# Kernel optimization log

Hardware: AMD Instinct MI355X
Metric: run time of the kernel (lower is better)

The kernel has to match this reference:

```python
import jax, jax.numpy as jnp
import numpy as np

B, T, HID = 4, 2048, 1024
H, FD, HD = 16, 16, 64          # heads, feature_dim, head_dim
CHUNK = 64                      # chunk size for chunked linear attention
EPS_LN = 1e-5                   # layer-norm eps inside feature map
EPS_Z = 1e-10                   # normalize_output eps


def setup_inputs() -> dict:
    key = jax.random.key(0)
    ks = jax.random.split(key, 7)
    init = lambda k, shp: jax.random.normal(k, shp, jnp.float32) * (shp[-1] ** -0.5)
    return {
        "hidden_states": jax.random.normal(ks[0], (B, T, HID), jnp.float32),
        "Wq": init(ks[1], (H * FD, HID)),     # q_proj weight [out,in], no bias
        "Wk": init(ks[2], (H * FD, HID)),
        "Wv": init(ks[3], (H * HD, HID)),
        "Wo": init(ks[4], (H * HD, HID)),
        "gamma": jnp.ones((FD,), jnp.float32),  # RebasedFeatureMap layer-norm scale
        "beta": jnp.zeros((FD,), jnp.float32),  # RebasedFeatureMap layer-norm shift
    }


def _feature_map(x, gamma, beta):
    # layer_norm over feature_dim, then quadratic (outer-product) feature map.
    mu = x.mean(-1, keepdims=True)
    var = ((x - mu) ** 2).mean(-1, keepdims=True)
    xn = (x - mu) * jax.lax.rsqrt(var + EPS_LN) * gamma + beta
    d = xn.shape[-1]
    # [B,T,H,d] -> [B,T,H,d*d]
    x2 = (xn[..., :, None] * xn[..., None, :]).reshape(*xn.shape[:-1], d * d)
    return x2 * (d ** -0.5)


def _chunk_linear_attn(q, k, v):
    # Chunk-recurrent causal linear attention (simple GLA with no gates, scale=1).
    Bq, Tq, Hq, Kq = q.shape
    Vd = v.shape[-1]
    N = Tq // CHUNK
    # [B,T,H,D] -> [N,B,H,C,D] for scan over chunks
    to_chunks = lambda x: x.reshape(Bq, N, CHUNK, Hq, x.shape[-1]).transpose(1, 0, 3, 2, 4)
    qc, kc, vc = to_chunks(q), to_chunks(k), to_chunks(v)
    mask = jnp.tril(jnp.ones((CHUNK, CHUNK), bool))

    def step(state, xs):
        qb, kb, vb = xs  # [B,H,C,K], [B,H,C,K], [B,H,C,V]
        att = jnp.einsum('bhik,bhjk->bhij', qb, kb)
        att = jnp.where(mask, att, 0.0)
        o = jnp.einsum('bhij,bhjv->bhiv', att, vb) + jnp.einsum('bhik,bhkv->bhiv', qb, state)
        state = state + jnp.einsum('bhck,bhcv->bhkv', kb, vb)
        return state, o

    state0 = jnp.zeros((Bq, Hq, Kq, Vd), q.dtype)
    _, o = jax.lax.scan(step, state0, (qc, kc, vc))  # o: [N,B,H,C,V]
    o = o.transpose(1, 0, 3, 2, 4).reshape(Bq, Tq, Hq, Vd)
    # normalize_output: z_t = q_t . cumsum_{s<=t} k_s
    z = jnp.einsum('bthk,bthk->bth', q, jnp.cumsum(k, axis=1))[..., None]
    return o / (z + EPS_Z)


def reference(hidden_states, Wq, Wk, Wv, Wo, gamma, beta):
    Bh, Th, _ = hidden_states.shape
    q = (hidden_states @ Wq.T).reshape(Bh, Th, H, FD)
    k = (hidden_states @ Wk.T).reshape(Bh, Th, H, FD)
    v = (hidden_states @ Wv.T).reshape(Bh, Th, H, HD)
    qf = _feature_map(q, gamma, beta)  # [B,T,H,FD*FD]
    kf = _feature_map(k, gamma, beta)
    o = _chunk_linear_attn(qf, kf, v)  # [B,T,H,HD]
    o = o.reshape(Bh, Th, H * HD)
    return o @ Wo.T
```

## Files before the change

kernel.cpp:

```cpp
#include <hip/hip_runtime.h>

#define T_SEQ 2048
#define BATCH 4
#define NH 16
#define FDIM 16
#define HDIM 64
#define HIDDEN 1024
#define TOK (BATCH * T_SEQ)
#define CH 128
#define NCHUNK (T_SEQ / CH)
#define NBH (BATCH * NH)

#define QK_OFF   0u
#define VT_OFF   4194304u
#define SRAW_OFF 8388608u
#define SPRE_OFF 16777216u
#define MK_OFF   25165824u
#define OAB_OFF  25427968u
#define WQKV_OFF 29622272u
#define WO_OFF   30408704u
#define HSB_OFF  30932992u

typedef float f32x4 __attribute__((ext_vector_type(4)));
typedef short bf16x8 __attribute__((ext_vector_type(8)));
typedef unsigned short us8 __attribute__((ext_vector_type(8)));
typedef unsigned short us4 __attribute__((ext_vector_type(4)));
typedef unsigned int u32;

__device__ __forceinline__ unsigned short f2b(float f) {
  union { float f; unsigned u; } v; v.f = f;
  unsigned r = (v.u + 0x7FFFu + ((v.u >> 16) & 1u)) >> 16;
  return (unsigned short)r;
}
__device__ __forceinline__ float b2f(unsigned short h) {
  union { unsigned u; float f; } v; v.u = ((unsigned)h) << 16; return v.f;
}

__device__ __forceinline__ void gload_lds16(const void* g, void* l) {
  __builtin_amdgcn_global_load_lds(
      (const __attribute__((address_space(1))) u32*)g,
      (__attribute__((address_space(3))) u32*)l, 16, 0, 0);
}

__global__ __launch_bounds__(256) void conv_all(const float* __restrict__ hs,
                                                const float* __restrict__ Wq,
                                                const float* __restrict__ Wk,
                                                const float* __restrict__ Wv,
                                                const float* __restrict__ Wo,
                                                unsigned short* __restrict__ HSB,
                                                unsigned short* __restrict__ WQKVB,
                                                unsigned short* __restrict__ WOB) {
  int i = blockIdx.x * 256 + threadIdx.x;
  const float* src;
  unsigned short* dst;
  if (i < 1048576) {
    int f = i * 8; src = hs + f; dst = HSB + f;
  } else if (i < 1245184) {
    int f = (i - 1048576) * 8;
    if (f < 262144)      src = Wq + f;
    else if (f < 524288) src = Wk + (f - 262144);
    else                 src = Wv + (f - 524288);
    dst = WQKVB + f;
  } else {
    int f = (i - 1245184) * 8;
    src = Wo + f; dst = WOB + f;
  }
  float4 v0 = *(const float4*)src, v1 = *(const float4*)(src + 4);
  us8 o;
  o[0] = f2b(v0.x); o[1] = f2b(v0.y); o[2] = f2b(v0.z); o[3] = f2b(v0.w);
  o[4] = f2b(v1.x); o[5] = f2b(v1.y); o[6] = f2b(v1.z); o[7] = f2b(v1.w);
  *(us8*)dst = o;
}

#define LDSA(p) (lds + (p) * 8192)
#define LDSB(p) (lds + 24576 + (p) * 16384)

__device__ __forceinline__ void stage6(const unsigned short* __restrict__ A,
                                       const unsigned short* __restrict__ B,
                                       int m0, int n0, int kt,
                                       unsigned short* ldsA, unsigned short* ldsB,
                                       int w, int lrow, int kswz) {
  const int kc = kt * 64 + kswz;
#pragma unroll
  for (int i = 0; i < 2; ++i) {
    int c = i * 8 + w;
    gload_lds16(&A[(size_t)(m0 + c * 8 + lrow) * HIDDEN + kc], &ldsA[c * 512]);
  }
#pragma unroll
  for (int i = 0; i < 4; ++i) {
    int c = i * 8 + w;
    gload_lds16(&B[(size_t)(n0 + c * 8 + lrow) * HIDDEN + kc], &ldsB[c * 512]);
  }
}

__device__ __forceinline__ void compute_tile(const unsigned short* __restrict__ ldsA,
                                             const unsigned short* __restrict__ ldsB,
                                             int wm, int wn, int ln, int lg,
                                             f32x4 acc[4][4]) {
  const int swz = (ln & 7) << 3;
#pragma unroll
  for (int kk = 0; kk < 2; ++kk) {
    const int col = (kk * 32 + lg * 8) ^ swz;
    bf16x8 af[4], bfr[4];
#pragma unroll
    for (int fm = 0; fm < 4; ++fm)
      af[fm] = *(const bf16x8*)&ldsA[(wm * 64 + fm * 16 + ln) * 64 + col];
#pragma unroll
    for (int fn = 0; fn < 4; ++fn)
      bfr[fn] = *(const bf16x8*)&ldsB[(wn * 64 + fn * 16 + ln) * 64 + col];
    __builtin_amdgcn_s_setprio(1);
#pragma unroll
    for (int fm = 0; fm < 4; ++fm)
#pragma unroll
      for (int fn = 0; fn < 4; ++fn)
        acc[fm][fn] = __builtin_amdgcn_mfma_f32_16x16x32_bf16(af[fm], bfr[fn], acc[fm][fn], 0, 0, 0);
    __builtin_amdgcn_s_setprio(0);
  }
}

#define GEMM_PIPELINE(Aptr, Bptr)                                              \
  const int tid = threadIdx.x;                                                 \
  const int lane = tid & 63, w = tid >> 6;                                     \
  const int wm = w >> 2, wn = w & 3;                                           \
  const int ln = lane & 15, lg = lane >> 4;                                    \
  const int lrow = lane >> 3;                                                  \
  const int kswz = (((lane & 7) ^ ((lane >> 3) & 7)) * 8);                     \
  f32x4 acc[4][4];                                                             \
  _Pragma("unroll") for (int m = 0; m < 4; ++m)                                \
    _Pragma("unroll") for (int n = 0; n < 4; ++n)                              \
      acc[m][n] = (f32x4){0.f, 0.f, 0.f, 0.f};                                 \
  stage6(Aptr, Bptr, m0, n0, 0, LDSA(0), LDSB(0), w, lrow, kswz);              \
  stage6(Aptr, Bptr, m0, n0, 1, LDSA(1), LDSB(1), w, lrow, kswz);              \
  int cur = 0;                                                                 \
  for (int t = 0; t < 16; ++t) {                                               \
    if (t < 14) {                                                              \
      int sb = cur + 2; if (sb >= 3) sb -= 3;                                  \
      stage6(Aptr, Bptr, m0, n0, t + 2, LDSA(sb), LDSB(sb), w, lrow, kswz);    \
      asm volatile("s_waitcnt vmcnt(12)" ::: "memory");                        \
    } else if (t == 14) {                                                      \
      asm volatile("s_waitcnt vmcnt(6)" ::: "memory");                         \
    } else {                                                                   \
      asm volatile("s_waitcnt vmcnt(0)" ::: "memory");                         \
    }                                                                          \
    __builtin_amdgcn_s_barrier();                                              \
    asm volatile("" ::: "memory");                                             \
    compute_tile(LDSA(cur), LDSB(cur), wm, wn, ln, lg, acc);                   \
    asm volatile("" ::: "memory");                                             \
    __builtin_amdgcn_s_barrier();                                              \
    cur = cur + 1; if (cur == 3) cur = 0;                                      \
  }

__global__ __launch_bounds__(512) void proj_gemm(const unsigned short* __restrict__ A,
                                                 const unsigned short* __restrict__ Wb,
                                                 float* __restrict__ QK,
                                                 unsigned short* __restrict__ VTg) {
  __shared__ unsigned short lds[73728];
  const int bid = blockIdx.x;
  const int logical = (bid & 7) * 48 + (bid >> 3);
  const int bx = logical / 6, by = logical % 6;
  const int m0 = bx * 128, n0 = by * 256;

  GEMM_PIPELINE(A, Wb)

  if (by < 2) {
#pragma unroll
    for (int fm = 0; fm < 4; ++fm)
#pragma unroll
      for (int fn = 0; fn < 4; ++fn) {
        int col = n0 + wn * 64 + fn * 16 + ln;
        int row0 = m0 + wm * 64 + fm * 16 + lg * 4;
#pragma unroll
        for (int j = 0; j < 4; ++j)
          QK[(size_t)(row0 + j) * 512 + col] = acc[fm][fn][j];
      }
  } else {
    unsigned short (*ct)[136] = (unsigned short(*)[136])lds;
#pragma unroll
    for (int fm = 0; fm < 4; ++fm)
#pragma unroll
      for (int fn = 0; fn < 4; ++fn) {
        int cl = wn * 64 + fn * 16 + ln;
        int r0 = wm * 64 + fm * 16 + lg * 4;
        us4 p;
#pragma unroll
        for (int j = 0; j < 4; ++j) p[j] = f2b(acc[fm][fn][j]);
        *(us4*)&ct[cl][r0] = p;
      }
    __builtin_amdgcn_s_barrier();
    asm volatile("" ::: "memory");
    const int vbase = n0 - 512;
    const int b = m0 >> 11, t0 = m0 & 2047;
#pragma unroll
    for (int it = 0; it < 8; ++it) {
      int sid = it * 512 + tid, vl = sid >> 4, tc = sid & 15;
      int vg = vbase + vl, h = vg >> 6, vd = vg & 63;
      us8 val = *(const us8*)&ct[vl][tc * 8];
      *(us8*)&VTg[(((size_t)(b * 16 + h) * 64 + vd) << 11) + t0 + tc * 8] = val;
    }
  }
}

__global__ __launch_bounds__(512) void out_gemm(const unsigned short* __restrict__ A,
                                                const unsigned short* __restrict__ W,
                                                float* __restrict__ C) {
  __shared__ unsigned short lds[73728];
  const int bid = blockIdx.x;
  const int logical = (bid & 7) * 32 + (bid >> 3);
  const int bx = logical >> 2, by = logical & 3;
  const int m0 = bx * 128, n0 = by * 256;

  GEMM_PIPELINE(A, W)

#pragma unroll
  for (int fm = 0; fm < 4; ++fm)
#pragma unroll
    for (int fn = 0; fn < 4; ++fn) {
      int col = n0 + wn * 64 + fn * 16 + ln;
      int row0 = m0 + wm * 64 + fm * 16 + lg * 4;
#pragma unroll
      for (int j = 0; j < 4; ++j)
        C[(size_t)(row0 + j) * 1024 + col] = acc[fm][fn][j];
    }
}

__device__ __forceinline__ void ln16(const float* __restrict__ src,
                                     const float* __restrict__ gamma,
                                     const float* __restrict__ beta,
                                     float* dst) {
  float x[16];
#pragma unroll
  for (int q = 0; q < 4; ++q) {
    float4 v = *(const float4*)(src + q * 4);
    x[q * 4 + 0] = v.x; x[q * 4 + 1] = v.y;
    x[q * 4 + 2] = v.z; x[q * 4 + 3] = v.w;
  }
  float mu = 0.f;
#pragma unroll
  for (int f = 0; f < 16; ++f) mu += x[f];
  mu *= 0.0625f;
  float var = 0.f;
#pragma unroll
  for (int f = 0; f < 16; ++f) { float d = x[f] - mu; var += d * d; }
  var *= 0.0625f;
  const float rs = rsqrtf(var + 1e-5f);
#pragma unroll
  for (int f = 0; f < 16; ++f) dst[f] = (x[f] - mu) * rs * gamma[f] + beta[f];
}

__global__ __launch_bounds__(256) void k_states(const float* __restrict__ QK,
                                                const unsigned short* __restrict__ VTg,
                                                const float* __restrict__ gamma,
                                                const float* __restrict__ beta,
                                                unsigned short* __restrict__ Sraw,
                                                float* __restrict__ Mk) {
  const int c = blockIdx.x, bh = blockIdx.y;
  const int b = bh >> 4, h = bh & 15;
  __shared__ float XKT[16][140];
  __shared__ unsigned short VT[64][152];
  const int tid = threadIdx.x;
  const int lane = tid & 63, wid = tid >> 6;
  const int ln = lane & 15, lg = lane >> 4;

  if (tid < 128) {
    float xr[16];
    ln16(QK + (size_t)(b * T_SEQ + c * CH + tid) * 512 + 256 + h * FDIM, gamma, beta, xr);
#pragma unroll
    for (int f = 0; f < 16; ++f) XKT[f][tid] = xr[f];
  }
#pragma unroll
  for (int it = 0; it < 4; ++it) {
    int flat = tid + it * 256; int v = flat >> 4, sb = flat & 15;
    *(us8*)&VT[v][sb * 8] = *(const us8*)&VTg[((size_t)bh * 64 + v) * T_SEQ + c * CH + sb * 8];
  }
  __syncthreads();

  {
    int i = tid >> 4, j = tid & 15;
    float m = 0.f;
    for (int cc = 0; cc < CH; ++cc) m += XKT[i][cc] * XKT[j][cc];
    Mk[((size_t)bh * NCHUNK + c) * 256 + tid] = m;
  }

  f32x4 acc[4][4];
#pragma unroll
  for (int m = 0; m < 4; ++m)
#pragma unroll
    for (int n = 0; n < 4; ++n) acc[m][n] = (f32x4){0.f, 0.f, 0.f, 0.f};

#pragma unroll
  for (int kt = 0; kt < 4; ++kt) {
    const int s0 = kt * 32 + lg * 8;
    bf16x8 bfr[4];
#pragma unroll
    for (int nt = 0; nt < 4; ++nt) bfr[nt] = *(const bf16x8*)&VT[nt * 16 + ln][s0];
#pragma unroll
    for (int mi = 0; mi < 4; ++mi) {
      const int iidx = wid * 4 + mi;
      float4 xi0 = *(const float4*)&XKT[iidx][s0];
      float4 xi1 = *(const float4*)&XKT[iidx][s0 + 4];
      float4 xj0 = *(const float4*)&XKT[ln][s0];
      float4 xj1 = *(const float4*)&XKT[ln][s0 + 4];
      bf16x8 afr;
      afr[0] = (short)f2b(xi0.x * xj0.x); afr[1] = (short)f2b(xi0.y * xj0.y);
      afr[2] = (short)f2b(xi0.z * xj0.z); afr[3] = (short)f2b(xi0.w * xj0.w);
      afr[4] = (short)f2b(xi1.x * xj1.x); afr[5] = (short)f2b(xi1.y * xj1.y);
      afr[6] = (short)f2b(xi1.z * xj1.z); afr[7] = (short)f2b(xi1.w * xj1.w);
#pragma unroll
      for (int nt = 0; nt < 4; ++nt)
        acc[mi][nt] = __builtin_amdgcn_mfma_f32_16x16x32_bf16(afr, bfr[nt], acc[mi][nt], 0, 0, 0);
    }
  }

  unsigned short* Sp = Sraw + ((size_t)bh * NCHUNK + c) * (64 * 256);
#pragma unroll
  for (int mi = 0; mi < 4; ++mi) {
    int r0 = (wid * 4 + mi) * 16 + lg * 4;
#pragma unroll
    for (int nt = 0; nt < 4; ++nt) {
      int n = nt * 16 + ln;
      us4 pk;
#pragma unroll
      for (int j = 0; j < 4; ++j) pk[j] = f2b(acc[mi][nt][j]);
      *(us4*)&Sp[(size_t)n * 256 + r0] = pk;
    }
  }
}

__global__ __launch_bounds__(256) void k_prefix(const unsigned short* __restrict__ Sraw,
                                                unsigned short* __restrict__ Spre,
                                                float* __restrict__ Mk) {
  const int bh = blockIdx.y;
  if (blockIdx.x < 8) {
    const int e8 = blockIdx.x * 256 + threadIdx.x;
    size_t base = (size_t)bh * NCHUNK * 16384 + (size_t)e8 * 8;
    float run[8] = {0.f, 0.f, 0.f, 0.f, 0.f, 0.f, 0.f, 0.f};
    for (int cc = 0; cc < NCHUNK; ++cc) {
      us8 v = *(const us8*)&Sraw[base + (size_t)cc * 16384];
      us8 w;
#pragma unroll
      for (int q = 0; q < 8; ++q) w[q] = f2b(run[q]);
      *(us8*)&Spre[base + (size_t)cc * 16384] = w;
#pragma unroll
      for (int q = 0; q < 8; ++q) run[q] += b2f(v[q]);
    }
  } else {
    const int e = threadIdx.x;
    size_t base = (size_t)bh * NCHUNK * 256 + e;
    float run = 0.f;
    for (int c = 0; c < NCHUNK; ++c) {
      float v = Mk[base + (size_t)c * 256];
      Mk[base + (size_t)c * 256] = run;
      run += v;
    }
  }
}

__global__ __launch_bounds__(256) void k_attn_out(const float* __restrict__ QK,
                                                  const unsigned short* __restrict__ VTg,
                                                  const float* __restrict__ gamma,
                                                  const float* __restrict__ beta,
                                                  const unsigned short* __restrict__ Spre,
                                                  const float* __restrict__ Mkp,
                                                  unsigned short* __restrict__ OAB) {
  const int c = blockIdx.x, bh = blockIdx.y;
  const int b = bh >> 4, h = bh & 15;
  __shared__ unsigned short XQb[128][40];
  __shared__ unsigned short XKb[128][40];
  __shared__ unsigned short attb[128 * 128];
  __shared__ unsigned short VT[64][152];
  __shared__ float mksh[256];
  const int tid = threadIdx.x;
  const int lane = tid & 63, wid = tid >> 6;
  const int ln = lane & 15, lg = lane >> 4;

  {
    int r = tid & 127;
    const float* src = QK + (size_t)(b * T_SEQ + c * CH + r) * 512 + (tid < 128 ? 0 : 256) + h * FDIM;
    unsigned short* dst = (tid < 128) ? &XQb[r][0] : &XKb[r][0];
    float xr[16];
    ln16(src, gamma, beta, xr);
    us8 lo, hi, z8;
#pragma unroll
    for (int q = 0; q < 8; ++q) { lo[q] = f2b(xr[q]); hi[q] = f2b(xr[8 + q]); z8[q] = 0; }
    *(us8*)&dst[0] = lo; *(us8*)&dst[8] = hi;
    *(us8*)&dst[16] = z8; *(us8*)&dst[24] = z8;
  }
#pragma unroll
  for (int it = 0; it < 4; ++it) {
    int flat = tid + it * 256; int v = flat >> 4, sb = flat & 15;
    *(us8*)&VT[v][sb * 8] = *(const us8*)&VTg[((size_t)bh * 64 + v) * T_SEQ + c * CH + sb * 8];
  }
  mksh[tid] = Mkp[((size_t)bh * NCHUNK + c) * 256 + tid];
  __syncthreads();

  const int tb = wid * 32;
  const f32x4 zero4 = {0.f, 0.f, 0.f, 0.f};

  bf16x8 aq0 = *(const bf16x8*)&XQb[tb + ln][lg * 8];
  bf16x8 aq1 = *(const bf16x8*)&XQb[tb + 16 + ln][lg * 8];
  float zin[2][4];
#pragma unroll
  for (int mt = 0; mt < 2; ++mt)
#pragma unroll
    for (int j = 0; j < 4; ++j) zin[mt][j] = 0.f;

#pragma unroll
  for (int nt = 0; nt < 8; ++nt) {
    bf16x8 bk = *(const bf16x8*)&XKb[nt * 16 + ln][lg * 8];
    f32x4 c0 = __builtin_amdgcn_mfma_f32_16x16x32_bf16(aq0, bk, zero4, 0, 0, 0);
    f32x4 c1 = __builtin_amdgcn_mfma_f32_16x16x32_bf16(aq1, bk, zero4, 0, 0, 0);
    int s = nt * 16 + ln;
#pragma unroll
    for (int j = 0; j < 4; ++j) {
      int t0 = tb + lg * 4 + j;
      float d0 = c0[j];
      float a0 = (s <= t0) ? d0 * d0 * 0.0625f : 0.f;
      zin[0][j] += a0;
      attb[t0 * 128 + (s ^ ((t0 & 7) << 3))] = f2b(a0);
      int t1 = t0 + 16;
      float d1 = c1[j];
      float a1 = (s <= t1) ? d1 * d1 * 0.0625f : 0.f;
      zin[1][j] += a1;
      attb[t1 * 128 + (s ^ ((t1 & 7) << 3))] = f2b(a1);
    }
  }
#pragma unroll
  for (int mt = 0; mt < 2; ++mt)
#pragma unroll
    for (int j = 0; j < 4; ++j) {
      float zz = zin[mt][j];
      zz += __shfl_xor(zz, 1, 64);
      zz += __shfl_xor(zz, 2, 64);
      zz += __shfl_xor(zz, 4, 64);
      zz += __shfl_xor(zz, 8, 64);
      zin[mt][j] = zz;
    }

  f32x4 o[2][4];
#pragma unroll
  for (int mt = 0; mt < 2; ++mt)
#pragma unroll
    for (int nt = 0; nt < 4; ++nt) o[mt][nt] = zero4;

#pragma unroll
  for (int kt = 0; kt < 4; ++kt) {
    int s0 = kt * 32 + lg * 8;
    bf16x8 a0 = *(const bf16x8*)&attb[(tb + ln) * 128 + (s0 ^ ((ln & 7) << 3))];
    bf16x8 a1 = *(const bf16x8*)&attb[(tb + 16 + ln) * 128 + (s0 ^ ((ln & 7) << 3))];
#pragma unroll
    for (int nt = 0; nt < 4; ++nt) {
      bf16x8 bv = *(const bf16x8*)&VT[nt * 16 + ln][s0];
      o[0][nt] = __builtin_amdgcn_mfma_f32_16x16x32_bf16(a0, bv, o[0][nt], 0, 0, 0);
      o[1][nt] = __builtin_amdgcn_mfma_f32_16x16x32_bf16(a1, bv, o[1][nt], 0, 0, 0);
    }
  }

  const unsigned short* Sp = Spre + ((size_t)bh * NCHUNK + c) * (64 * 256);
  bf16x8 xlo0 = *(const bf16x8*)&XQb[tb + ln][0];
  bf16x8 xhi0 = *(const bf16x8*)&XQb[tb + ln][8];
  bf16x8 xlo1 = *(const bf16x8*)&XQb[tb + 16 + ln][0];
  bf16x8 xhi1 = *(const bf16x8*)&XQb[tb + 16 + ln][8];
#pragma unroll
  for (int kt = 0; kt < 8; ++kt) {
    int i = kt * 2 + (lg >> 1);
    float xqi0 = b2f(XQb[tb + ln][i]) * 0.0625f;
    float xqi1 = b2f(XQb[tb + 16 + ln][i]) * 0.0625f;
    bf16x8 sel0 = (lg & 1) ? xhi0 : xlo0;
    bf16x8 sel1 = (lg & 1) ? xhi1 : xlo1;
    bf16x8 qa0, qa1;
#pragma unroll
    for (int jj = 0; jj < 8; ++jj) {
      qa0[jj] = (short)f2b(xqi0 * b2f((unsigned short)sel0[jj]));
      qa1[jj] = (short)f2b(xqi1 * b2f((unsigned short)sel1[jj]));
    }
    int r0 = kt * 32 + lg * 8;
#pragma unroll
    for (int nt = 0; nt < 4; ++nt) {
      bf16x8 bp = *(const bf16x8*)&Sp[(size_t)(nt * 16 + ln) * 256 + r0];
      o[0][nt] = __builtin_amdgcn_mfma_f32_16x16x32_bf16(qa0, bp, o[0][nt], 0, 0, 0);
      o[1][nt] = __builtin_amdgcn_mfma_f32_16x16x32_bf16(qa1, bp, o[1][nt], 0, 0, 0);
    }
  }

  float zi2[2][4];
#pragma unroll
  for (int mt = 0; mt < 2; ++mt)
#pragma unroll
    for (int j = 0; j < 4; ++j) {
      int t = tb + mt * 16 + lg * 4 + j;
      float xqi = b2f(XQb[t][ln]);
      float p = 0.f;
#pragma unroll
      for (int jm = 0; jm < 16; ++jm) p += b2f(XQb[t][jm]) * mksh[jm * 16 + ln];
      p *= xqi;
      p += __shfl_xor(p, 1, 64);
      p += __shfl_xor(p, 2, 64);
      p += __shfl_xor(p, 4, 64);
      p += __shfl_xor(p, 8, 64);
      zi2[mt][j] = p * 0.0625f;
    }

  unsigned short* ob = OAB + ((size_t)(b * T_SEQ + c * CH)) * 1024 + h * 64;
#pragma unroll
  for (int mt = 0; mt < 2; ++mt)
#pragma unroll
    for (int j = 0; j < 4; ++j) {
      int t = tb + mt * 16 + lg * 4 + j;
      float inv = 1.0f / (zin[mt][j] + zi2[mt][j] + 1e-10f);
#pragma unroll
      for (int nt = 0; nt < 4; ++nt)
        ob[(size_t)t * 1024 + nt * 16 + ln] = f2b(o[mt][nt][j] * inv);
    }
}

extern "C" void kernel_launch(void* const* d_in, const int* in_sizes, int n_in,
                              void* d_out, int out_size, void* d_ws, size_t ws_size,
                              hipStream_t stream) {
  const float* hs    = (const float*)d_in[0];
  const float* Wq    = (const float*)d_in[1];
  const float* Wk    = (const float*)d_in[2];
  const float* Wv    = (const float*)d_in[3];
  const float* Wo    = (const float*)d_in[4];
  const float* gamma = (const float*)d_in[5];
  const float* beta  = (const float*)d_in[6];
  float* out = (float*)d_out;
  float* ws  = (float*)d_ws;

  float* QK = ws + QK_OFF;
  unsigned short* VTg   = (unsigned short*)(ws + VT_OFF);
  unsigned short* Sraw  = (unsigned short*)(ws + SRAW_OFF);
  unsigned short* Spre  = (unsigned short*)(ws + SPRE_OFF);
  float* Mk = ws + MK_OFF;
  unsigned short* OAB   = (unsigned short*)(ws + OAB_OFF);
  unsigned short* WQKVB = (unsigned short*)(ws + WQKV_OFF);
  unsigned short* WOB   = (unsigned short*)(ws + WO_OFF);
  unsigned short* HSB   = (unsigned short*)(ws + HSB_OFF);

  dim3 blk(256);
  conv_all<<<5376, blk, 0, stream>>>(hs, Wq, Wk, Wv, Wo, HSB, WQKVB, WOB);
  proj_gemm<<<384, dim3(512), 0, stream>>>(HSB, WQKVB, QK, VTg);
  k_states<<<dim3(NCHUNK, NBH), blk, 0, stream>>>(QK, VTg, gamma, beta, Sraw, Mk);
  k_prefix<<<dim3(9, NBH), blk, 0, stream>>>(Sraw, Spre, Mk);
  k_attn_out<<<dim3(NCHUNK, NBH), blk, 0, stream>>>(QK, VTg, gamma, beta, Spre, Mk, OAB);
  out_gemm<<<256, dim3(512), 0, stream>>>(OAB, WOB, out);
}
```

Measured before the change: 137.7 us.

## Restructure GEMM main loop into four interleaved quadrant phases with split staging

Replaces the per-k-tile stage-then-compute loop with a schedule that splits each tile into four MFMA quadrants. LDS fragment reads, global-to-LDS stage issues and barriers are interleaved between the quadrants so memory traffic overlaps with matrix work at a finer grain. This adds many extra block barriers per iteration and tighter vmcnt bookkeeping. Each barrier can stall the waves, and a miscounted wait could race on LDS buffers.

```diff
diff --git a/kernel.cpp b/kernel.cpp
--- a/kernel.cpp
+++ b/kernel.cpp
@@ -75,79 +75,103 @@
 #define LDSA(p) (lds + (p) * 8192)
 #define LDSB(p) (lds + 24576 + (p) * 16384)
 
-__device__ __forceinline__ void stage6(const unsigned short* __restrict__ A,
-                                       const unsigned short* __restrict__ B,
-                                       int m0, int n0, int kt,
-                                       unsigned short* ldsA, unsigned short* ldsB,
-                                       int w, int lrow, int kswz) {
+__device__ __forceinline__ void stageA2(const unsigned short* __restrict__ A,
+                                        int m0, int kt, unsigned short* ldsA,
+                                        int w, int lrow, int kswz) {
   const int kc = kt * 64 + kswz;
-#pragma unroll
-  for (int i = 0; i < 2; ++i) {
-    int c = i * 8 + w;
-    gload_lds16(&A[(size_t)(m0 + c * 8 + lrow) * HIDDEN + kc], &ldsA[c * 512]);
-  }
-#pragma unroll
-  for (int i = 0; i < 4; ++i) {
-    int c = i * 8 + w;
-    gload_lds16(&B[(size_t)(n0 + c * 8 + lrow) * HIDDEN + kc], &ldsB[c * 512]);
-  }
-}
-
-__device__ __forceinline__ void compute_tile(const unsigned short* __restrict__ ldsA,
-                                             const unsigned short* __restrict__ ldsB,
-                                             int wm, int wn, int ln, int lg,
-                                             f32x4 acc[4][4]) {
-  const int swz = (ln & 7) << 3;
-#pragma unroll
-  for (int kk = 0; kk < 2; ++kk) {
-    const int col = (kk * 32 + lg * 8) ^ swz;
-    bf16x8 af[4], bfr[4];
-#pragma unroll
-    for (int fm = 0; fm < 4; ++fm)
-      af[fm] = *(const bf16x8*)&ldsA[(wm * 64 + fm * 16 + ln) * 64 + col];
-#pragma unroll
-    for (int fn = 0; fn < 4; ++fn)
-      bfr[fn] = *(const bf16x8*)&ldsB[(wn * 64 + fn * 16 + ln) * 64 + col];
-    __builtin_amdgcn_s_setprio(1);
-#pragma unroll
-    for (int fm = 0; fm < 4; ++fm)
-#pragma unroll
-      for (int fn = 0; fn < 4; ++fn)
-        acc[fm][fn] = __builtin_amdgcn_mfma_f32_16x16x32_bf16(af[fm], bfr[fn], acc[fm][fn], 0, 0, 0);
-    __builtin_amdgcn_s_setprio(0);
-  }
-}
-
-#define GEMM_PIPELINE(Aptr, Bptr)                                              \
-  const int tid = threadIdx.x;                                                 \
-  const int lane = tid & 63, w = tid >> 6;                                     \
-  const int wm = w >> 2, wn = w & 3;                                           \
-  const int ln = lane & 15, lg = lane >> 4;                                    \
-  const int lrow = lane >> 3;                                                  \
-  const int kswz = (((lane & 7) ^ ((lane >> 3) & 7)) * 8);                     \
-  f32x4 acc[4][4];                                                             \
-  _Pragma("unroll") for (int m = 0; m < 4; ++m)                                \
-    _Pragma("unroll") for (int n = 0; n < 4; ++n)                              \
-      acc[m][n] = (f32x4){0.f, 0.f, 0.f, 0.f};                                 \
-  stage6(Aptr, Bptr, m0, n0, 0, LDSA(0), LDSB(0), w, lrow, kswz);              \
-  stage6(Aptr, Bptr, m0, n0, 1, LDSA(1), LDSB(1), w, lrow, kswz);              \
-  int cur = 0;                                                                 \
-  for (int t = 0; t < 16; ++t) {                                               \
-    if (t < 14) {                                                              \
-      int sb = cur + 2; if (sb >= 3) sb -= 3;                                  \
-      stage6(Aptr, Bptr, m0, n0, t + 2, LDSA(sb), LDSB(sb), w, lrow, kswz);    \
-      asm volatile("s_waitcnt vmcnt(12)" ::: "memory");                        \
-    } else if (t == 14) {                                                      \
-      asm volatile("s_waitcnt vmcnt(6)" ::: "memory");                         \
-    } else {                                                                   \
-      asm volatile("s_waitcnt vmcnt(0)" ::: "memory");                         \
-    }                                                                          \
-    __builtin_amdgcn_s_barrier();                                              \
-    asm volatile("" ::: "memory");                                             \
-    compute_tile(LDSA(cur), LDSB(cur), wm, wn, ln, lg, acc);                   \
-    asm volatile("" ::: "memory");                                             \
-    __builtin_amdgcn_s_barrier();                                              \
-    cur = cur + 1; if (cur == 3) cur = 0;                                      \
+  gload_lds16(&A[(size_t)(m0 + w * 8 + lrow) * HIDDEN + kc], &ldsA[w * 512]);
+  gload_lds16(&A[(size_t)(m0 + 64 + w * 8 + lrow) * HIDDEN + kc], &ldsA[(8 + w) * 512]);
+}
+__device__ __forceinline__ void stageB1(const unsigned short* __restrict__ B,
+                                        int n0, int kt, unsigned short* ldsB,
+                                        int i, int w, int lrow, int kswz) {
+  const int kc = kt * 64 + kswz;
+  const int c = i * 8 + w;
+  gload_lds16(&B[(size_t)(n0 + c * 8 + lrow) * HIDDEN + kc], &ldsB[c * 512]);
+}
+
+#define BARF() do { asm volatile("" ::: "memory"); __builtin_amdgcn_s_barrier(); \
+                    asm volatile("" ::: "memory"); } while (0)
+
+#define RD_A(fm, kk) (*(const bf16x8*)&cA[(wm * 64 + (fm) * 16 + ln) * 64 + (((kk) * 32 + lg * 8) ^ swz)])
+#define RD_B(fn, kk) (*(const bf16x8*)&cB[(wn * 64 + (fn) * 16 + ln) * 64 + (((kk) * 32 + lg * 8) ^ swz)])
+
+#define MFMA_Q(fmA, fmB, fnA, fnB, aA0, aA1, aB0, aB1, bA0, bA1, bB0, bB1)       \
+  __builtin_amdgcn_s_setprio(1);                                                  \
+  acc[fmA][fnA] = __builtin_amdgcn_mfma_f32_16x16x32_bf16(aA0, bA0, acc[fmA][fnA], 0, 0, 0); \
+  acc[fmA][fnA] = __builtin_amdgcn_mfma_f32_16x16x32_bf16(aA1, bA1, acc[fmA][fnA], 0, 0, 0); \
+  acc[fmA][fnB] = __builtin_amdgcn_mfma_f32_16x16x32_bf16(aA0, bB0, acc[fmA][fnB], 0, 0, 0); \
+  acc[fmA][fnB] = __builtin_amdgcn_mfma_f32_16x16x32_bf16(aA1, bB1, acc[fmA][fnB], 0, 0, 0); \
+  acc[fmB][fnA] = __builtin_amdgcn_mfma_f32_16x16x32_bf16(aB0, bA0, acc[fmB][fnA], 0, 0, 0); \
+  acc[fmB][fnA] = __builtin_amdgcn_mfma_f32_16x16x32_bf16(aB1, bA1, acc[fmB][fnA], 0, 0, 0); \
+  acc[fmB][fnB] = __builtin_amdgcn_mfma_f32_16x16x32_bf16(aB0, bB0, acc[fmB][fnB], 0, 0, 0); \
+  acc[fmB][fnB] = __builtin_amdgcn_mfma_f32_16x16x32_bf16(aB1, bB1, acc[fmB][fnB], 0, 0, 0); \
+  __builtin_amdgcn_s_setprio(0);
+
+#define GEMM_PIPELINE(Aptr, Bptr)                                                \
+  const int tid = threadIdx.x;                                                   \
+  const int lane = tid & 63, w = tid >> 6;                                       \
+  const int wm = w >> 2, wn = w & 3;                                             \
+  const int ln = lane & 15, lg = lane >> 4;                                      \
+  const int lrow = lane >> 3;                                                    \
+  const int kswz = (((lane & 7) ^ ((lane >> 3) & 7)) * 8);                       \
+  const int swz = (ln & 7) << 3;                                                 \
+  f32x4 acc[4][4];                                                               \
+  _Pragma("unroll") for (int m = 0; m < 4; ++m)                                  \
+    _Pragma("unroll") for (int n = 0; n < 4; ++n)                                \
+      acc[m][n] = (f32x4){0.f, 0.f, 0.f, 0.f};                                   \
+  stageA2(Aptr, m0, 0, LDSA(0), w, lrow, kswz);                                  \
+  stageB1(Bptr, n0, 0, LDSB(0), 0, w, lrow, kswz);                               \
+  stageB1(Bptr, n0, 0, LDSB(0), 1, w, lrow, kswz);                               \
+  stageB1(Bptr, n0, 0, LDSB(0), 2, w, lrow, kswz);                               \
+  stageB1(Bptr, n0, 0, LDSB(0), 3, w, lrow, kswz);                               \
+  stageA2(Aptr, m0, 1, LDSA(1), w, lrow, kswz);                                  \
+  stageB1(Bptr, n0, 1, LDSB(1), 0, w, lrow, kswz);                               \
+  stageB1(Bptr, n0, 1, LDSB(1), 1, w, lrow, kswz);                               \
+  stageB1(Bptr, n0, 1, LDSB(1), 2, w, lrow, kswz);                               \
+  stageB1(Bptr, n0, 1, LDSB(1), 3, w, lrow, kswz);                               \
+  asm volatile("s_waitcnt vmcnt(6)" ::: "memory");                               \
+  __builtin_amdgcn_s_barrier();                                                  \
+  int cur = 0;                                                                   \
+  _Pragma("unroll 1") for (int t = 0; t < 16; ++t) {                             \
+    const unsigned short* cA = LDSA(cur);                                        \
+    const unsigned short* cB = LDSB(cur);                                        \
+    int sb = cur + 2; if (sb >= 3) sb -= 3;                                      \
+    unsigned short* nA = LDSA(sb);                                               \
+    unsigned short* nB = LDSB(sb);                                               \
+    const bool st = (t <= 13);                                                   \
+                                           \
+    bf16x8 a0_0 = RD_A(0, 0), a0_1 = RD_A(0, 1);                                 \
+    bf16x8 a1_0 = RD_A(1, 0), a1_1 = RD_A(1, 1);                                 \
+    bf16x8 b0_0 = RD_B(0, 0), b0_1 = RD_B(0, 1);                                 \
+    bf16x8 b1_0 = RD_B(1, 0), b1_1 = RD_B(1, 1);                                 \
+    if (st) stageA2(Aptr, m0, t + 2, nA, w, lrow, kswz);                         \
+    BARF();                                                                      \
+    MFMA_Q(0, 1, 0, 1, a0_0, a0_1, a1_0, a1_1, b0_0, b0_1, b1_0, b1_1)           \
+    BARF();                                                                      \
+                                            \
+    bf16x8 b2_0 = RD_B(2, 0), b2_1 = RD_B(2, 1);                                 \
+    bf16x8 b3_0 = RD_B(3, 0), b3_1 = RD_B(3, 1);                                 \
+    if (st) { stageB1(Bptr, n0, t + 2, nB, 0, w, lrow, kswz);                    \
+              stageB1(Bptr, n0, t + 2, nB, 1, w, lrow, kswz); }                  \
+    BARF();                                                                      \
+    MFMA_Q(0, 1, 2, 3, a0_0, a0_1, a1_0, a1_1, b2_0, b2_1, b3_0, b3_1)           \
+    BARF();                                                                      \
+                                               \
+    bf16x8 a2_0 = RD_A(2, 0), a2_1 = RD_A(2, 1);                                 \
+    bf16x8 a3_0 = RD_A(3, 0), a3_1 = RD_A(3, 1);                                 \
+    if (st) stageB1(Bptr, n0, t + 2, nB, 2, w, lrow, kswz);                      \
+    BARF();                                                                      \
+    MFMA_Q(2, 3, 2, 3, a2_0, a2_1, a3_0, a3_1, b2_0, b2_1, b3_0, b3_1)           \
+    BARF();                                                                      \
+                        \
+    if (st) stageB1(Bptr, n0, t + 2, nB, 3, w, lrow, kswz);                      \
+    if (t < 14) { asm volatile("s_waitcnt vmcnt(6)" ::: "memory"); }             \
+    else if (t == 14) { asm volatile("s_waitcnt vmcnt(0)" ::: "memory"); }       \
+    BARF();                                                                      \
+    MFMA_Q(2, 3, 0, 1, a2_0, a2_1, a3_0, a3_1, b0_0, b0_1, b1_0, b1_1)           \
+    BARF();                                                                      \
+    cur = cur + 1; if (cur == 3) cur = 0;                                        \
   }
 
 __global__ __launch_bounds__(512) void proj_gemm(const unsigned short* __restrict__ A,
@@ -186,8 +210,7 @@
         for (int j = 0; j < 4; ++j) p[j] = f2b(acc[fm][fn][j]);
         *(us4*)&ct[cl][r0] = p;
       }
-    __builtin_amdgcn_s_barrier();
-    asm volatile("" ::: "memory");
+    BARF();
     const int vbase = n0 - 512;
     const int b = m0 >> 11, t0 = m0 & 2047;
 #pragma unroll
```

Result: no change. 137.6 us (-0.1%).

## Restructure projection GEMMs to 128x128 tiles with double-buffered register-prefetch pipeline

Applied to the files above, without the earlier changes.

Both bf16 GEMMs move from 128x256 tiles with 512 threads and a triple-buffered LDS ring to 128x128 tiles with 256 threads (4 waves, each computing 64x64) and a two-buffer LDS scheme. Each iteration reads all fragments of the current stage into registers, synchronises, then issues the global->LDS load of stage t+2 into the same buffer while the MFMAs run. Grids double, LDS per block drops, and occupancy and wave count per CU change. The intent is better latency hiding and more blocks per CU, at the cost of lower per-block arithmetic intensity and more register pressure from holding 16 fragments.

```diff
diff --git a/kernel.cpp b/kernel.cpp
--- a/kernel.cpp
+++ b/kernel.cpp
@@ -73,96 +73,83 @@
 }
 
 #define LDSA(p) (lds + (p) * 8192)
-#define LDSB(p) (lds + 24576 + (p) * 16384)
-
-__device__ __forceinline__ void stage6(const unsigned short* __restrict__ A,
+#define LDSB(p) (lds + 16384 + (p) * 8192)
+
+__device__ __forceinline__ void stage8(const unsigned short* __restrict__ A,
                                        const unsigned short* __restrict__ B,
                                        int m0, int n0, int kt,
-                                       unsigned short* ldsA, unsigned short* ldsB,
+                                       unsigned short* lA, unsigned short* lB,
                                        int w, int lrow, int kswz) {
   const int kc = kt * 64 + kswz;
 #pragma unroll
-  for (int i = 0; i < 2; ++i) {
-    int c = i * 8 + w;
-    gload_lds16(&A[(size_t)(m0 + c * 8 + lrow) * HIDDEN + kc], &ldsA[c * 512]);
-  }
-#pragma unroll
   for (int i = 0; i < 4; ++i) {
-    int c = i * 8 + w;
-    gload_lds16(&B[(size_t)(n0 + c * 8 + lrow) * HIDDEN + kc], &ldsB[c * 512]);
-  }
-}
-
-__device__ __forceinline__ void compute_tile(const unsigned short* __restrict__ ldsA,
-                                             const unsigned short* __restrict__ ldsB,
-                                             int wm, int wn, int ln, int lg,
-                                             f32x4 acc[4][4]) {
-  const int swz = (ln & 7) << 3;
-#pragma unroll
-  for (int kk = 0; kk < 2; ++kk) {
-    const int col = (kk * 32 + lg * 8) ^ swz;
-    bf16x8 af[4], bfr[4];
-#pragma unroll
-    for (int fm = 0; fm < 4; ++fm)
-      af[fm] = *(const bf16x8*)&ldsA[(wm * 64 + fm * 16 + ln) * 64 + col];
-#pragma unroll
-    for (int fn = 0; fn < 4; ++fn)
-      bfr[fn] = *(const bf16x8*)&ldsB[(wn * 64 + fn * 16 + ln) * 64 + col];
-    __builtin_amdgcn_s_setprio(1);
-#pragma unroll
-    for (int fm = 0; fm < 4; ++fm)
-#pragma unroll
-      for (int fn = 0; fn < 4; ++fn)
-        acc[fm][fn] = __builtin_amdgcn_mfma_f32_16x16x32_bf16(af[fm], bfr[fn], acc[fm][fn], 0, 0, 0);
-    __builtin_amdgcn_s_setprio(0);
-  }
-}
+    int r = w * 32 + i * 8;
+    gload_lds16(&A[(size_t)(m0 + r + lrow) * HIDDEN + kc], &lA[r * 64]);
+  }
+#pragma unroll
+  for (int i = 0; i < 4; ++i) {
+    int r = w * 32 + i * 8;
+    gload_lds16(&B[(size_t)(n0 + r + lrow) * HIDDEN + kc], &lB[r * 64]);
+  }
+}
+
+#define RD_A(fm, kk) (*(const bf16x8*)&cA[(wm * 64 + (fm) * 16 + ln) * 64 + (((kk) * 32 + lg * 8) ^ swz)])
+#define RD_B(fn, kk) (*(const bf16x8*)&cB[(wn * 64 + (fn) * 16 + ln) * 64 + (((kk) * 32 + lg * 8) ^ swz)])
 
 #define GEMM_PIPELINE(Aptr, Bptr)                                              \
   const int tid = threadIdx.x;                                                 \
   const int lane = tid & 63, w = tid >> 6;                                     \
-  const int wm = w >> 2, wn = w & 3;                                           \
+  const int wm = w >> 1, wn = w & 1;                                           \
   const int ln = lane & 15, lg = lane >> 4;                                    \
   const int lrow = lane >> 3;                                                  \
   const int kswz = (((lane & 7) ^ ((lane >> 3) & 7)) * 8);                     \
+  const int swz = (ln & 7) << 3;                                               \
   f32x4 acc[4][4];                                                             \
   _Pragma("unroll") for (int m = 0; m < 4; ++m)                                \
     _Pragma("unroll") for (int n = 0; n < 4; ++n)                              \
       acc[m][n] = (f32x4){0.f, 0.f, 0.f, 0.f};                                 \
-  stage6(Aptr, Bptr, m0, n0, 0, LDSA(0), LDSB(0), w, lrow, kswz);              \
-  stage6(Aptr, Bptr, m0, n0, 1, LDSA(1), LDSB(1), w, lrow, kswz);              \
-  int cur = 0;                                                                 \
-  for (int t = 0; t < 16; ++t) {                                               \
-    if (t < 14) {                                                              \
-      int sb = cur + 2; if (sb >= 3) sb -= 3;                                  \
-      stage6(Aptr, Bptr, m0, n0, t + 2, LDSA(sb), LDSB(sb), w, lrow, kswz);    \
-      asm volatile("s_waitcnt vmcnt(12)" ::: "memory");                        \
-    } else if (t == 14) {                                                      \
-      asm volatile("s_waitcnt vmcnt(6)" ::: "memory");                         \
-    } else {                                                                   \
-      asm volatile("s_waitcnt vmcnt(0)" ::: "memory");                         \
+  stage8(Aptr, Bptr, m0, n0, 0, LDSA(0), LDSB(0), w, lrow, kswz);              \
+  stage8(Aptr, Bptr, m0, n0, 1, LDSA(1), LDSB(1), w, lrow, kswz);              \
+  asm volatile("s_waitcnt vmcnt(8)" ::: "memory");                             \
+  __builtin_amdgcn_s_barrier();                                                \
+  _Pragma("unroll 1") for (int t = 0; t < 16; ++t) {                           \
+    const unsigned short* cA = LDSA(t & 1);                                    \
+    const unsigned short* cB = LDSB(t & 1);                                    \
+    bf16x8 af[4][2], bfr[4][2];                                                \
+    _Pragma("unroll") for (int f = 0; f < 4; ++f) {                            \
+      af[f][0] = RD_A(f, 0); af[f][1] = RD_A(f, 1);                            \
+      bfr[f][0] = RD_B(f, 0); bfr[f][1] = RD_B(f, 1);                          \
     }                                                                          \
+    asm volatile("s_waitcnt lgkmcnt(0)" ::: "memory");                         \
+    __builtin_amdgcn_sched_barrier(0);                                         \
     __builtin_amdgcn_s_barrier();                                              \
-    asm volatile("" ::: "memory");                                             \
-    compute_tile(LDSA(cur), LDSB(cur), wm, wn, ln, lg, acc);                   \
-    asm volatile("" ::: "memory");                                             \
+    if (t <= 13)                                                               \
+      stage8(Aptr, Bptr, m0, n0, t + 2, LDSA(t & 1), LDSB(t & 1), w, lrow, kswz); \
+    __builtin_amdgcn_s_setprio(1);                                             \
+    _Pragma("unroll") for (int kk = 0; kk < 2; ++kk)                           \
+      _Pragma("unroll") for (int fm = 0; fm < 4; ++fm)                         \
+        _Pragma("unroll") for (int fn = 0; fn < 4; ++fn)                       \
+          acc[fm][fn] = __builtin_amdgcn_mfma_f32_16x16x32_bf16(               \
+              af[fm][kk], bfr[fn][kk], acc[fm][fn], 0, 0, 0);                  \
+    __builtin_amdgcn_s_setprio(0);                                             \
+    if (t <= 13) { asm volatile("s_waitcnt vmcnt(8)" ::: "memory"); }          \
+    else if (t == 14) { asm volatile("s_waitcnt vmcnt(0)" ::: "memory"); }     \
     __builtin_amdgcn_s_barrier();                                              \
-    cur = cur + 1; if (cur == 3) cur = 0;                                      \
-  }
-
-__global__ __launch_bounds__(512) void proj_gemm(const unsigned short* __restrict__ A,
+  }
+
+__global__ __launch_bounds__(256) void proj_gemm(const unsigned short* __restrict__ A,
                                                  const unsigned short* __restrict__ Wb,
                                                  float* __restrict__ QK,
                                                  unsigned short* __restrict__ VTg) {
-  __shared__ unsigned short lds[73728];
+  __shared__ unsigned short lds[32768];
   const int bid = blockIdx.x;
-  const int logical = (bid & 7) * 48 + (bid >> 3);
-  const int bx = logical / 6, by = logical % 6;
-  const int m0 = bx * 128, n0 = by * 256;
+  const int logical = (bid & 7) * 96 + (bid >> 3);
+  const int bx = logical / 12, by = logical % 12;
+  const int m0 = bx * 128, n0 = by * 128;
 
   GEMM_PIPELINE(A, Wb)
 
-  if (by < 2) {
+  if (by < 4) {
 #pragma unroll
     for (int fm = 0; fm < 4; ++fm)
 #pragma unroll
@@ -192,7 +179,7 @@
     const int b = m0 >> 11, t0 = m0 & 2047;
 #pragma unroll
     for (int it = 0; it < 8; ++it) {
-      int sid = it * 512 + tid, vl = sid >> 4, tc = sid & 15;
+      int sid = it * 256 + tid, vl = sid >> 4, tc = sid & 15;
       int vg = vbase + vl, h = vg >> 6, vd = vg & 63;
       us8 val = *(const us8*)&ct[vl][tc * 8];
       *(us8*)&VTg[(((size_t)(b * 16 + h) * 64 + vd) << 11) + t0 + tc * 8] = val;
@@ -200,14 +187,14 @@
   }
 }
 
-__global__ __launch_bounds__(512) void out_gemm(const unsigned short* __restrict__ A,
+__global__ __launch_bounds__(256) void out_gemm(const unsigned short* __restrict__ A,
                                                 const unsigned short* __restrict__ W,
                                                 float* __restrict__ C) {
-  __shared__ unsigned short lds[73728];
+  __shared__ unsigned short lds[32768];
   const int bid = blockIdx.x;
-  const int logical = (bid & 7) * 32 + (bid >> 3);
-  const int bx = logical >> 2, by = logical & 3;
-  const int m0 = bx * 128, n0 = by * 256;
+  const int logical = (bid & 7) * 64 + (bid >> 3);
+  const int bx = logical >> 3, by = logical & 7;
+  const int m0 = bx * 128, n0 = by * 128;
 
   GEMM_PIPELINE(A, W)
 
@@ -538,9 +525,9 @@
 
   dim3 blk(256);
   conv_all<<<5376, blk, 0, stream>>>(hs, Wq, Wk, Wv, Wo, HSB, WQKVB, WOB);
-  proj_gemm<<<384, dim3(512), 0, stream>>>(HSB, WQKVB, QK, VTg);
+  proj_gemm<<<768, blk, 0, stream>>>(HSB, WQKVB, QK, VTg);
   k_states<<<dim3(NCHUNK, NBH), blk, 0, stream>>>(QK, VTg, gamma, beta, Sraw, Mk);
   k_prefix<<<dim3(9, NBH), blk, 0, stream>>>(Sraw, Spre, Mk);
   k_attn_out<<<dim3(NCHUNK, NBH), blk, 0, stream>>>(QK, VTg, gamma, beta, Spre, Mk, OAB);
-  out_gemm<<<256, dim3(512), 0, stream>>>(OAB, WOB, out);
-}
+  out_gemm<<<512, blk, 0, stream>>>(OAB, WOB, out);
+}
```

New measurement: 127.4 us. 7.4% less time.
